# Kernel tuning notes

Measured on AMD Instinct MI355X. Metric: run time of the kernel, lower is better.

The kernel has to match this reference:

```python
import jax, jax.numpy as jnp
import numpy as np

SHAPE = 64
K = 8
HID = 512
OUT = K + 2 * K * SHAPE + 2 * SHAPE  # 1160
B, T = 32, 2048


def setup_inputs() -> dict:
    key = jax.random.key(0)
    ks = jax.random.split(key, 4)
    x = jax.random.normal(ks[0], (B, T, SHAPE), dtype=jnp.float32)
    W1 = jax.random.normal(ks[1], (SHAPE, HID), dtype=jnp.float32) / np.sqrt(SHAPE)
    b1 = jnp.zeros((HID,), dtype=jnp.float32)
    W2 = jax.random.normal(ks[2], (HID, HID), dtype=jnp.float32) / np.sqrt(HID)
    b2 = jnp.zeros((HID,), dtype=jnp.float32)
    W3 = jax.random.normal(ks[3], (HID, OUT), dtype=jnp.float32) / np.sqrt(HID) * 0.1
    b3 = jnp.zeros((OUT,), dtype=jnp.float32)
    return {"x": x, "W1": W1, "b1": b1, "W2": W2, "b2": b2, "W3": W3, "b3": b3}


def _coupling_forward(x, W1, b1, W2, b2, W3, b3):
    # coupling mask over feature dim: first half conditions the second half
    mask = jnp.zeros((SHAPE,), dtype=x.dtype).at[:SHAPE // 2].set(1.0)  # [D]
    x_ = x * mask  # [B,T,D]

    # conditioner MLP
    h = jax.nn.relu(x_ @ W1 + b1)
    h = jax.nn.relu(h @ W2 + b2)
    params = h @ W3 + b3  # [B,T,OUT]

    logscales = params[..., :SHAPE]
    biases = params[..., SHAPE:2 * SHAPE]
    mdn = params[..., 2 * SHAPE:]
    logits = mdn[..., :K]                                   # [B,T,K]
    mu = mdn[..., K:K + K * SHAPE].reshape(*x.shape[:2], K, SHAPE)
    logstd = mdn[..., K + K * SHAPE:].reshape(*x.shape[:2], K, SHAPE)

    # --- MixtureCDFFlow.flow ---
    weights = jax.nn.softmax(logits, axis=-1)[..., None]    # [B,T,K,1]
    std = jnp.exp(logstd)
    u = (x[:, :, None, :] - mu) / std                       # [B,T,K,D]
    cdf = 0.5 * (1.0 + jax.lax.erf(u / np.sqrt(2.0)))
    z = jnp.sum(cdf * weights, axis=2)                      # [B,T,D]
    pdf = jnp.exp(-0.5 * u * u) / (std * np.sqrt(2.0 * np.pi))
    logd_mix = jnp.log(jnp.sum(pdf * weights, axis=2))      # [B,T,D]

    # --- Inverse(Sigmoid).flow == Sigmoid.invert ---
    xs = -jnp.log(1.0 / z - 1.0)
    logd_sig = -jnp.log(z) - jnp.log(1.0 - z)

    # --- ElemwiseAffine.flow ---
    out = xs * jnp.exp(logscales) + biases
    log_det = logd_mix + logd_sig + logscales

    x_out = (1.0 - mask) * out + x_
    log_det = log_det * (1.0 - mask)
    return x_out, log_det


def reference(x, W1, b1, W2, b2, W3, b3):
    return _coupling_forward(x, W1, b1, W2, b2, W3, b3)
```

## Files before the change

kernel.cpp:

```cpp
#include <hip/hip_runtime.h>

typedef short short8 __attribute__((ext_vector_type(8)));
typedef float f32x4 __attribute__((ext_vector_type(4)));

#define NROWS 65536
#define NCOMPACT 640

__device__ __forceinline__ short f2bf(float f) {
  union { float f; unsigned u; } c; c.f = f;
  unsigned r = (c.u + 0x7fffu + ((c.u >> 16) & 1u)) >> 16;
  return (short)r;
}

__device__ __forceinline__ float fastrcp(float a) {
  float r; asm("v_rcp_f32 %0, %1" : "=v"(r) : "v"(a)); return r;
}

__device__ __forceinline__ int w3col(int n) {
  if (n < 32)  return 32 + n;
  if (n < 64)  return 96 + (n - 32);
  if (n < 72)  return 128 + (n - 64);
  if (n < 96)  return -1;
  if (n < 352) { int q = n - 96;  return 168 + (q >> 5) * 64 + (q & 31); }
  if (n < 608) { int q = n - 352; return 680 + (q >> 5) * 64 + (q & 31); }
  return -1;
}

__global__ __launch_bounds__(256) void prep_x_kernel(const float* __restrict__ x,
                                                     short* __restrict__ xc) {
  int t = blockIdx.x * 256 + threadIdx.x;
  if (t >= NROWS * 4) return;
  int row = t >> 2, seg = t & 3;
  const float* src = x + (size_t)row * 64 + seg * 8;
  short8 v;
#pragma unroll
  for (int i = 0; i < 8; ++i) v[i] = f2bf(src[i]);
  *(short8*)(xc + (size_t)row * 32 + seg * 8) = v;
}

__global__ __launch_bounds__(256) void prep_w_kernel(
    const float* __restrict__ W1, const float* __restrict__ W2,
    const float* __restrict__ W3, const float* __restrict__ b3,
    short* __restrict__ w1t, short* __restrict__ w2t,
    short* __restrict__ w3t, float* __restrict__ b3c) {
  const int NW1 = 512 * 32, NW2 = 512 * 512, NW3 = NCOMPACT * 512;
  int t = blockIdx.x * 256 + threadIdx.x;
  if (t < NW1) {
    int n = t >> 5, k = t & 31;
    w1t[t] = f2bf(W1[k * 512 + n]);
  } else if (t < NW1 + NW2) {
    int i = t - NW1; int n = i >> 9, k = i & 511;
    w2t[i] = f2bf(W2[k * 512 + n]);
  } else if (t < NW1 + NW2 + NW3) {
    int i = t - NW1 - NW2; int n = i >> 9, k = i & 511;
    int c = w3col(n);
    w3t[i] = (c >= 0) ? f2bf(W3[(size_t)k * 1160 + c]) : (short)0;
  } else if (t < NW1 + NW2 + NW3 + NCOMPACT) {
    int n = t - NW1 - NW2 - NW3;
    int c = w3col(n);
    b3c[n] = (c >= 0) ? b3[c] : 0.0f;
  }
}

template <int BK, int NT, bool RELU, bool OUT_BF16>
__global__ __launch_bounds__(256) void gemm_kernel(
    const short* __restrict__ A, const short* __restrict__ B,
    const float* __restrict__ bias, void* __restrict__ C, int K, int N) {
  __shared__ short As[128 * BK];
  __shared__ short Bs[128 * BK];
  const int tid = threadIdx.x;
  const int cpx = gridDim.x >> 3;
  const int s = blockIdx.x;
  const int w = (s & 7) * cpx + (s >> 3);
  const int m0 = (w / NT) * 128, n0 = (w % NT) * 128;
  const int lane = tid & 63, wid = tid >> 6;
  const int wm = (wid >> 1) * 64, wn = (wid & 1) * 64;
  const int lr = lane & 15, lk = (lane >> 4) * 8;
  constexpr int CPR = BK / 8;
  constexpr int SWM = CPR - 1;
  constexpr int NCHUNK = 128 * CPR;

  f32x4 acc[4][4] = {};

  for (int kt = 0; kt < K; kt += BK) {
    for (int base = wid * 64; base < NCHUNK; base += 256) {
      int c = base + lane;
      int row = c / CPR;
      int kb = (c % CPR) << 4;
      int skb = kb ^ ((row & SWM) << 4);
      const char* ga = (const char*)(A + (size_t)(m0 + row) * K + kt) + skb;
      const char* gb = (const char*)(B + (size_t)(n0 + row) * K + kt) + skb;
      __builtin_amdgcn_global_load_lds(
          (const __attribute__((address_space(1))) void*)ga,
          (__attribute__((address_space(3))) void*)((char*)As + (size_t)base * 16), 16, 0, 0);
      __builtin_amdgcn_global_load_lds(
          (const __attribute__((address_space(1))) void*)gb,
          (__attribute__((address_space(3))) void*)((char*)Bs + (size_t)base * 16), 16, 0, 0);
    }
    __syncthreads();
#pragma unroll
    for (int ks = 0; ks < BK; ks += 32) {
      short8 af[4], bf_[4];
#pragma unroll
      for (int mi = 0; mi < 4; ++mi) {
        int row = wm + mi * 16 + lr;
        int k = (ks + lk) ^ ((row & SWM) << 3);
        af[mi] = *(const short8*)(&As[row * BK + k]);
      }
#pragma unroll
      for (int ni = 0; ni < 4; ++ni) {
        int row = wn + ni * 16 + lr;
        int k = (ks + lk) ^ ((row & SWM) << 3);
        bf_[ni] = *(const short8*)(&Bs[row * BK + k]);
      }
#pragma unroll
      for (int mi = 0; mi < 4; ++mi)
#pragma unroll
        for (int ni = 0; ni < 4; ++ni)
          acc[mi][ni] = __builtin_amdgcn_mfma_f32_16x16x32_bf16(
              af[mi], bf_[ni], acc[mi][ni], 0, 0, 0);
    }
    __syncthreads();
  }

#pragma unroll
  for (int ni = 0; ni < 4; ++ni) {
    int col = n0 + wn + ni * 16 + lr;
    float bv = bias[col];
#pragma unroll
    for (int mi = 0; mi < 4; ++mi) {
#pragma unroll
      for (int j = 0; j < 4; ++j) {
        int row = m0 + wm + mi * 16 + (lane >> 4) * 4 + j;
        float v = acc[mi][ni][j] + bv;
        if (RELU) v = fmaxf(v, 0.0f);
        if (OUT_BF16) ((short*)C)[(size_t)row * N + col] = f2bf(v);
        else          ((float*)C)[(size_t)row * N + col] = v;
      }
    }
  }
}

#define PSTR 644
#define BUF1 49152
__global__ __launch_bounds__(1024, 4) void gemm3_fused_kernel(
    const short* __restrict__ A,
    const short* __restrict__ Bw,
    const float* __restrict__ b3c,
    const float* __restrict__ x,
    float* __restrict__ out) {
  __shared__ __attribute__((aligned(16))) char lds[98304];
  const int tid = threadIdx.x;
  const int m0 = blockIdx.x * 128;
  const int lane = tid & 63, wid = tid >> 6;
  const int wr = wid >> 2, wc = wid & 3;
  const int lr = lane & 15, hi = lane >> 4, lk = hi * 8;

  f32x4 acc[2][10] = {};

  auto STAGE = [&](int bo, int kt) {
#pragma unroll
    for (int base = wid * 64; base < 3072; base += 1024) {
      int c = base + lane;
      char* dst = lds + bo + (size_t)base * 16;
      if (base < 512) {
        int row = c >> 2;
        int skb = ((c & 3) ^ ((row >> 1) & 3)) << 4;
        const char* ga = (const char*)(A + (size_t)(m0 + row) * 512 + kt) + skb;
        __builtin_amdgcn_global_load_lds(
            (const __attribute__((address_space(1))) void*)ga,
            (__attribute__((address_space(3))) void*)dst, 16, 0, 0);
      } else {
        int q = c - 512;
        int row = q >> 2;
        int skb = ((q & 3) ^ ((row >> 1) & 3)) << 4;
        const char* gb = (const char*)(Bw + (size_t)row * 512 + kt) + skb;
        __builtin_amdgcn_global_load_lds(
            (const __attribute__((address_space(1))) void*)gb,
            (__attribute__((address_space(3))) void*)dst, 16, 0, 0);
      }
    }
  };

  auto COMPUTE = [&](int bo) {
    const short* As = (const short*)(lds + bo);
    const short* Bs = (const short*)(lds + bo + 8192);
    short8 af[2];
#pragma unroll
    for (int mi = 0; mi < 2; ++mi) {
      int row = wr * 32 + mi * 16 + lr;
      int k = lk ^ (((row >> 1) & 3) << 3);
      af[mi] = *(const short8*)(&As[row * 32 + k]);
    }
#pragma unroll
    for (int ni = 0; ni < 10; ++ni) {
      int brow = wc * 160 + ni * 16 + lr;
      int k = lk ^ (((brow >> 1) & 3) << 3);
      short8 bf_ = *(const short8*)(&Bs[brow * 32 + k]);
      acc[0][ni] = __builtin_amdgcn_mfma_f32_16x16x32_bf16(af[0], bf_, acc[0][ni], 0, 0, 0);
      acc[1][ni] = __builtin_amdgcn_mfma_f32_16x16x32_bf16(af[1], bf_, acc[1][ni], 0, 0, 0);
    }
  };

  STAGE(0, 0);
  __syncthreads();
  for (int t = 0; t < 16; t += 2) {
    STAGE(BUF1, (t + 1) * 32);
    COMPUTE(0);
    __syncthreads();
    if (t < 14) STAGE(0, (t + 2) * 32);
    COMPUTE(BUF1);
    __syncthreads();
  }

  float* plds = (float*)lds;
  float* xo  = out;
  float* ldo = out + (size_t)NROWS * 64;
#pragma unroll
  for (int p = 0; p < 4; ++p) {
    if (p) __syncthreads();
    if (wr == p) {
#pragma unroll
      for (int mi = 0; mi < 2; ++mi) {
#pragma unroll
        for (int ni = 0; ni < 10; ++ni) {
          int col = wc * 160 + ni * 16 + lr;
          float bv = b3c[col];
#pragma unroll
          for (int j = 0; j < 4; ++j)
            plds[(mi * 16 + hi * 4 + j) * PSTR + col] = acc[mi][ni][j] + bv;
        }
      }
    }
    __syncthreads();
    {
      int rl = tid >> 5, j = tid & 31;
      const float* p_ = plds + rl * PSTR;
      int grow = m0 + p * 32 + rl;

      float lg[8];
#pragma unroll
      for (int k = 0; k < 8; ++k) lg[k] = p_[64 + k];
      float mx = lg[0];
#pragma unroll
      for (int k = 1; k < 8; ++k) mx = fmaxf(mx, lg[k]);
      float wgt[8], wsum = 0.0f;
#pragma unroll
      for (int k = 0; k < 8; ++k) { wgt[k] = __expf(lg[k] - mx); wsum += wgt[k]; }

      float xd = x[(size_t)grow * 64 + 32 + j];
      float zs = 0.0f, ps = 0.0f;
#pragma unroll
      for (int k = 0; k < 8; ++k) {
        float mu   = p_[96 + k * 32 + j];
        float lstd = p_[352 + k * 32 + j];
        float istd = __expf(-lstd);
        float u = (xd - mu) * istd;
        float x2 = 0.5f * u * u;
        float e  = __expf(-x2);
        ps += wgt[k] * e * istd;
        float ax = fabsf(u) * 0.70710678118654752f;
        float t_ = fastrcp(fmaf(0.5f, ax, 1.0f));
        float poly = -1.26551223f + t_*(1.00002368f + t_*(0.37409196f +
                     t_*(0.09678418f + t_*(-0.18628806f + t_*(0.27886807f +
                     t_*(-1.13520398f + t_*(1.48851587f + t_*(-0.82215223f +
                     t_*0.17087277f))))))));
        float erfc_half = 0.5f * t_ * __expf(poly - x2);
        float cdf = (u >= 0.0f) ? 1.0f - erfc_half : erfc_half;
        zs += wgt[k] * cdf;
      }
      float winv = fastrcp(wsum);
      float z  = zs * winv;
      float pm = ps * winv * 0.39894228040143268f;
      float logz = __logf(z), log1mz = __logf(1.0f - z);
      float ls = p_[j], bv = p_[32 + j];
      float outv = (logz - log1mz) * __expf(ls) + bv;
      float ld = __logf(pm) - logz - log1mz + ls;

      size_t base = (size_t)grow * 64;
      xo[base + j]       = x[base + j];
      xo[base + 32 + j]  = outv;
      ldo[base + j]      = 0.0f;
      ldo[base + 32 + j] = ld;
    }
  }
}

extern "C" void kernel_launch(void* const* d_in, const int* in_sizes, int n_in,
                              void* d_out, int out_size, void* d_ws, size_t ws_size,
                              hipStream_t stream) {
  const float* x  = (const float*)d_in[0];
  const float* W1 = (const float*)d_in[1];
  const float* b1 = (const float*)d_in[2];
  const float* W2 = (const float*)d_in[3];
  const float* b2 = (const float*)d_in[4];
  const float* W3 = (const float*)d_in[5];
  const float* b3 = (const float*)d_in[6];
  char* ws = (char*)d_ws;

  short* xc  = (short*)ws;
  short* h1  = (short*)(ws + 4194304);
  short* h2  = (short*)(ws + 71303168);
  short* w1t = (short*)(ws + 138412032);
  short* w2t = (short*)(ws + 138444800);
  short* w3t = (short*)(ws + 138969088);
  float* b3c = (float*)(ws + 139624448);
  float* out = (float*)d_out;

  prep_x_kernel<<<(NROWS * 4) / 256, 256, 0, stream>>>(x, xc);
  {
    int total = 512 * 32 + 512 * 512 + NCOMPACT * 512 + NCOMPACT;
    prep_w_kernel<<<(total + 255) / 256, 256, 0, stream>>>(W1, W2, W3, b3, w1t, w2t, w3t, b3c);
  }
  gemm_kernel<32, 4, true, true><<<2048, 256, 0, stream>>>(xc, w1t, b1, h1, 32, 512);
  gemm_kernel<64, 4, true, true><<<2048, 256, 0, stream>>>(h1, w2t, b2, h2, 512, 512);
  gemm3_fused_kernel<<<NROWS / 128, 1024, 0, stream>>>(h2, w3t, b3c, x, out);
}
```

Measured before the change: 145.2 us.

## Reshape warp tiling to 2x8 and pipeline GEMM3 with vmcnt waits

Changes the fused third GEMM's wave layout from 4x4 to 2x8, so each wave computes a 64x80 tile (4x5 MFMA fragments) instead of 32x160. The main loop now keeps two LDS stages in flight. It uses explicit vmcnt waits and raw s_barriers instead of __syncthreads, and wraps the MFMA section in s_setprio. The goal is to overlap global-to-LDS loads with MFMA work and rebalance LDS fragment reads. The catch is fragile hand-managed wait counts and a different accumulator register footprint.

```diff
diff --git a/kernel.cpp b/kernel.cpp
--- a/kernel.cpp
+++ b/kernel.cpp
@@ -142,7 +142,8 @@
 }
 
 #define PSTR 644
-#define BUF1 49152
+#define FB1 49152
+#define WAITV(n) asm volatile("s_waitcnt vmcnt(" #n ")" ::: "memory")
 __global__ __launch_bounds__(1024, 4) void gemm3_fused_kernel(
     const short* __restrict__ A,
     const short* __restrict__ Bw,
@@ -153,10 +154,10 @@
   const int tid = threadIdx.x;
   const int m0 = blockIdx.x * 128;
   const int lane = tid & 63, wid = tid >> 6;
-  const int wr = wid >> 2, wc = wid & 3;
+  const int wr = wid >> 3, wc = wid & 7;
   const int lr = lane & 15, hi = lane >> 4, lk = hi * 8;
 
-  f32x4 acc[2][10] = {};
+  f32x4 acc[4][5] = {};
 
   auto STAGE = [&](int bo, int kt) {
 #pragma unroll
@@ -185,33 +186,51 @@
   auto COMPUTE = [&](int bo) {
     const short* As = (const short*)(lds + bo);
     const short* Bs = (const short*)(lds + bo + 8192);
-    short8 af[2];
-#pragma unroll
-    for (int mi = 0; mi < 2; ++mi) {
-      int row = wr * 32 + mi * 16 + lr;
+    short8 af[4];
+#pragma unroll
+    for (int mi = 0; mi < 4; ++mi) {
+      int row = wr * 64 + mi * 16 + lr;
       int k = lk ^ (((row >> 1) & 3) << 3);
       af[mi] = *(const short8*)(&As[row * 32 + k]);
     }
-#pragma unroll
-    for (int ni = 0; ni < 10; ++ni) {
-      int brow = wc * 160 + ni * 16 + lr;
+    __builtin_amdgcn_s_setprio(1);
+#pragma unroll
+    for (int ni = 0; ni < 5; ++ni) {
+      int brow = wc * 80 + ni * 16 + lr;
       int k = lk ^ (((brow >> 1) & 3) << 3);
       short8 bf_ = *(const short8*)(&Bs[brow * 32 + k]);
-      acc[0][ni] = __builtin_amdgcn_mfma_f32_16x16x32_bf16(af[0], bf_, acc[0][ni], 0, 0, 0);
-      acc[1][ni] = __builtin_amdgcn_mfma_f32_16x16x32_bf16(af[1], bf_, acc[1][ni], 0, 0, 0);
-    }
+#pragma unroll
+      for (int mi = 0; mi < 4; ++mi)
+        acc[mi][ni] = __builtin_amdgcn_mfma_f32_16x16x32_bf16(
+            af[mi], bf_, acc[mi][ni], 0, 0, 0);
+    }
+    __builtin_amdgcn_s_setprio(0);
   };
 
   STAGE(0, 0);
+  STAGE(FB1, 32);
+  for (int t = 0; t < 14; ++t) {
+    WAITV(3);
+    __builtin_amdgcn_sched_barrier(0);
+    __builtin_amdgcn_s_barrier();
+    __builtin_amdgcn_sched_barrier(0);
+    COMPUTE((t & 1) ? FB1 : 0);
+    __builtin_amdgcn_sched_barrier(0);
+    __builtin_amdgcn_s_barrier();
+    __builtin_amdgcn_sched_barrier(0);
+    STAGE((t & 1) ? FB1 : 0, (t + 2) * 32);
+  }
+  WAITV(3);
+  __builtin_amdgcn_sched_barrier(0);
+  __builtin_amdgcn_s_barrier();
+  __builtin_amdgcn_sched_barrier(0);
+  COMPUTE(0);
+  WAITV(0);
+  __builtin_amdgcn_sched_barrier(0);
+  __builtin_amdgcn_s_barrier();
+  __builtin_amdgcn_sched_barrier(0);
+  COMPUTE(FB1);
   __syncthreads();
-  for (int t = 0; t < 16; t += 2) {
-    STAGE(BUF1, (t + 1) * 32);
-    COMPUTE(0);
-    __syncthreads();
-    if (t < 14) STAGE(0, (t + 2) * 32);
-    COMPUTE(BUF1);
-    __syncthreads();
-  }
 
   float* plds = (float*)lds;
   float* xo  = out;
@@ -219,16 +238,17 @@
 #pragma unroll
   for (int p = 0; p < 4; ++p) {
     if (p) __syncthreads();
-    if (wr == p) {
-#pragma unroll
-      for (int mi = 0; mi < 2; ++mi) {
-#pragma unroll
-        for (int ni = 0; ni < 10; ++ni) {
-          int col = wc * 160 + ni * 16 + lr;
+    if (wr == (p >> 1)) {
+#pragma unroll
+      for (int mi2 = 0; mi2 < 2; ++mi2) {
+#pragma unroll
+        for (int ni = 0; ni < 5; ++ni) {
+          int col = wc * 80 + ni * 16 + lr;
           float bv = b3c[col];
 #pragma unroll
           for (int j = 0; j < 4; ++j)
-            plds[(mi * 16 + hi * 4 + j) * PSTR + col] = acc[mi][ni][j] + bv;
+            plds[(mi2 * 16 + hi * 4 + j) * PSTR + col] =
+                acc[(p & 1) * 2 + mi2][ni][j] + bv;
         }
       }
     }
```

New measurement: 146.5 us. About the same (+0.9%).

## Fuse all three MLP layers and epilogue into one per-row-block megakernel

Applied to the files above, without the earlier changes.

Replaces the x-prep kernel, the two standalone GEMM kernels and the fused third GEMM with a single kernel. Each 64-row block converts x to bf16 in LDS, computes layer 1, keeps the hidden activations in swizzled LDS across layers 2 and 3, and streams weight tiles through double buffers. This removes the HBM round trips for the h1/h2 intermediates and several launches. In exchange each block uses about 148KB of LDS, so only one block fits per CU, and every block re-streams all the weights (with smaller M tiles), which lowers occupancy and reuse.

```diff
diff --git a/kernel.cpp b/kernel.cpp
--- a/kernel.cpp
+++ b/kernel.cpp
@@ -2,6 +2,7 @@
 
 typedef short short8 __attribute__((ext_vector_type(8)));
 typedef float f32x4 __attribute__((ext_vector_type(4)));
+typedef float f32x4v __attribute__((ext_vector_type(4)));
 
 #define NROWS 65536
 #define NCOMPACT 640
@@ -24,18 +25,6 @@
   if (n < 352) { int q = n - 96;  return 168 + (q >> 5) * 64 + (q & 31); }
   if (n < 608) { int q = n - 352; return 680 + (q >> 5) * 64 + (q & 31); }
   return -1;
-}
-
-__global__ __launch_bounds__(256) void prep_x_kernel(const float* __restrict__ x,
-                                                     short* __restrict__ xc) {
-  int t = blockIdx.x * 256 + threadIdx.x;
-  if (t >= NROWS * 4) return;
-  int row = t >> 2, seg = t & 3;
-  const float* src = x + (size_t)row * 64 + seg * 8;
-  short8 v;
-#pragma unroll
-  for (int i = 0; i < 8; ++i) v[i] = f2bf(src[i]);
-  *(short8*)(xc + (size_t)row * 32 + seg * 8) = v;
 }
 
 __global__ __launch_bounds__(256) void prep_w_kernel(
@@ -62,154 +51,152 @@
   }
 }
 
-template <int BK, int NT, bool RELU, bool OUT_BF16>
-__global__ __launch_bounds__(256) void gemm_kernel(
-    const short* __restrict__ A, const short* __restrict__ B,
-    const float* __restrict__ bias, void* __restrict__ C, int K, int N) {
-  __shared__ short As[128 * BK];
-  __shared__ short Bs[128 * BK];
+#define OFF_A 0
+#define OFF_B 4096
+#define OFF_C 45056
+#define OFF_H 86016
+#define PSTR 644
+
+__global__ __launch_bounds__(1024) void mega_kernel(
+    const float* __restrict__ x,
+    const short* __restrict__ w1t,
+    const float* __restrict__ b1,
+    const short* __restrict__ w2t,
+    const float* __restrict__ b2,
+    const short* __restrict__ w3t,
+    const float* __restrict__ b3c,
+    float* __restrict__ out) {
+  __shared__ __attribute__((aligned(16))) char lds[151552];
   const int tid = threadIdx.x;
-  const int cpx = gridDim.x >> 3;
-  const int s = blockIdx.x;
-  const int w = (s & 7) * cpx + (s >> 3);
-  const int m0 = (w / NT) * 128, n0 = (w % NT) * 128;
+  const int m0 = blockIdx.x * 64;
   const int lane = tid & 63, wid = tid >> 6;
-  const int wm = (wid >> 1) * 64, wn = (wid & 1) * 64;
-  const int lr = lane & 15, lk = (lane >> 4) * 8;
-  constexpr int CPR = BK / 8;
-  constexpr int SWM = CPR - 1;
-  constexpr int NCHUNK = 128 * CPR;
-
-  f32x4 acc[4][4] = {};
-
-  for (int kt = 0; kt < K; kt += BK) {
-    for (int base = wid * 64; base < NCHUNK; base += 256) {
+  const int wr = wid >> 3, wc = wid & 7;
+  const int lr = lane & 15, hi = lane >> 4, lk = hi * 8;
+  short* Hs = (short*)(lds + OFF_H);
+
+  auto STAGE_W = [&](int bo, const short* src, int stride, int kt, int nchunk) {
+    for (int base = wid * 64; base < nchunk; base += 1024) {
       int c = base + lane;
-      int row = c / CPR;
-      int kb = (c % CPR) << 4;
-      int skb = kb ^ ((row & SWM) << 4);
-      const char* ga = (const char*)(A + (size_t)(m0 + row) * K + kt) + skb;
-      const char* gb = (const char*)(B + (size_t)(n0 + row) * K + kt) + skb;
+      int row = c >> 2;
+      int skb = ((c & 3) ^ ((row >> 1) & 3)) << 4;
+      const char* g = (const char*)(src + (size_t)row * stride + kt) + skb;
       __builtin_amdgcn_global_load_lds(
-          (const __attribute__((address_space(1))) void*)ga,
-          (__attribute__((address_space(3))) void*)((char*)As + (size_t)base * 16), 16, 0, 0);
-      __builtin_amdgcn_global_load_lds(
-          (const __attribute__((address_space(1))) void*)gb,
-          (__attribute__((address_space(3))) void*)((char*)Bs + (size_t)base * 16), 16, 0, 0);
-    }
-    __syncthreads();
-#pragma unroll
-    for (int ks = 0; ks < BK; ks += 32) {
-      short8 af[4], bf_[4];
-#pragma unroll
-      for (int mi = 0; mi < 4; ++mi) {
-        int row = wm + mi * 16 + lr;
-        int k = (ks + lk) ^ ((row & SWM) << 3);
-        af[mi] = *(const short8*)(&As[row * BK + k]);
-      }
-#pragma unroll
-      for (int ni = 0; ni < 4; ++ni) {
-        int row = wn + ni * 16 + lr;
-        int k = (ks + lk) ^ ((row & SWM) << 3);
-        bf_[ni] = *(const short8*)(&Bs[row * BK + k]);
-      }
-#pragma unroll
-      for (int mi = 0; mi < 4; ++mi)
-#pragma unroll
-        for (int ni = 0; ni < 4; ++ni)
-          acc[mi][ni] = __builtin_amdgcn_mfma_f32_16x16x32_bf16(
-              af[mi], bf_[ni], acc[mi][ni], 0, 0, 0);
-    }
-    __syncthreads();
-  }
-
-#pragma unroll
-  for (int ni = 0; ni < 4; ++ni) {
-    int col = n0 + wn + ni * 16 + lr;
-    float bv = bias[col];
-#pragma unroll
-    for (int mi = 0; mi < 4; ++mi) {
-#pragma unroll
-      for (int j = 0; j < 4; ++j) {
-        int row = m0 + wm + mi * 16 + (lane >> 4) * 4 + j;
-        float v = acc[mi][ni][j] + bv;
-        if (RELU) v = fmaxf(v, 0.0f);
-        if (OUT_BF16) ((short*)C)[(size_t)row * N + col] = f2bf(v);
-        else          ((float*)C)[(size_t)row * N + col] = v;
-      }
-    }
-  }
-}
-
-#define PSTR 644
-#define BUF1 49152
-__global__ __launch_bounds__(1024, 4) void gemm3_fused_kernel(
-    const short* __restrict__ A,
-    const short* __restrict__ Bw,
-    const float* __restrict__ b3c,
-    const float* __restrict__ x,
-    float* __restrict__ out) {
-  __shared__ __attribute__((aligned(16))) char lds[98304];
-  const int tid = threadIdx.x;
-  const int m0 = blockIdx.x * 128;
-  const int lane = tid & 63, wid = tid >> 6;
-  const int wr = wid >> 2, wc = wid & 3;
-  const int lr = lane & 15, hi = lane >> 4, lk = hi * 8;
-
-  f32x4 acc[2][10] = {};
-
-  auto STAGE = [&](int bo, int kt) {
-#pragma unroll
-    for (int base = wid * 64; base < 3072; base += 1024) {
-      int c = base + lane;
-      char* dst = lds + bo + (size_t)base * 16;
-      if (base < 512) {
-        int row = c >> 2;
-        int skb = ((c & 3) ^ ((row >> 1) & 3)) << 4;
-        const char* ga = (const char*)(A + (size_t)(m0 + row) * 512 + kt) + skb;
-        __builtin_amdgcn_global_load_lds(
-            (const __attribute__((address_space(1))) void*)ga,
-            (__attribute__((address_space(3))) void*)dst, 16, 0, 0);
-      } else {
-        int q = c - 512;
-        int row = q >> 2;
-        int skb = ((q & 3) ^ ((row >> 1) & 3)) << 4;
-        const char* gb = (const char*)(Bw + (size_t)row * 512 + kt) + skb;
-        __builtin_amdgcn_global_load_lds(
-            (const __attribute__((address_space(1))) void*)gb,
-            (__attribute__((address_space(3))) void*)dst, 16, 0, 0);
-      }
+          (const __attribute__((address_space(1))) void*)g,
+          (__attribute__((address_space(3))) void*)(lds + bo + (size_t)base * 16),
+          16, 0, 0);
     }
   };
 
-  auto COMPUTE = [&](int bo) {
-    const short* As = (const short*)(lds + bo);
-    const short* Bs = (const short*)(lds + bo + 8192);
+  if (tid < 256) {
+    int row = tid >> 2, seg = tid & 3;
+    const float* src = x + (size_t)(m0 + row) * 64 + seg * 8;
+    f32x4 v0 = *(const f32x4*)src;
+    f32x4 v1 = *(const f32x4*)(src + 4);
+    short8 v;
+#pragma unroll
+    for (int i = 0; i < 4; ++i) { v[i] = f2bf(v0[i]); v[4 + i] = f2bf(v1[i]); }
+    int sseg = seg ^ ((row >> 1) & 3);
+    *(short8*)(lds + OFF_A + row * 64 + sseg * 16) = v;
+  }
+  STAGE_W(OFF_B, w1t, 32, 0, 2048);
+  __syncthreads();
+
+  {
+    const short* As = (const short*)(lds + OFF_A);
+    const short* Ws = (const short*)(lds + OFF_B);
+    f32x4 acc1[2][4] = {};
     short8 af[2];
 #pragma unroll
     for (int mi = 0; mi < 2; ++mi) {
       int row = wr * 32 + mi * 16 + lr;
-      int k = lk ^ (((row >> 1) & 3) << 3);
-      af[mi] = *(const short8*)(&As[row * 32 + k]);
-    }
-#pragma unroll
-    for (int ni = 0; ni < 10; ++ni) {
-      int brow = wc * 160 + ni * 16 + lr;
-      int k = lk ^ (((brow >> 1) & 3) << 3);
-      short8 bf_ = *(const short8*)(&Bs[brow * 32 + k]);
-      acc[0][ni] = __builtin_amdgcn_mfma_f32_16x16x32_bf16(af[0], bf_, acc[0][ni], 0, 0, 0);
-      acc[1][ni] = __builtin_amdgcn_mfma_f32_16x16x32_bf16(af[1], bf_, acc[1][ni], 0, 0, 0);
-    }
-  };
-
-  STAGE(0, 0);
+      af[mi] = *(const short8*)(&As[row * 32 + (lk ^ (((row >> 1) & 3) << 3))]);
+    }
+#pragma unroll
+    for (int ni = 0; ni < 4; ++ni) {
+      int brow = wc * 64 + ni * 16 + lr;
+      short8 bf_ = *(const short8*)(&Ws[brow * 32 + (lk ^ (((brow >> 1) & 3) << 3))]);
+      acc1[0][ni] = __builtin_amdgcn_mfma_f32_16x16x32_bf16(af[0], bf_, acc1[0][ni], 0, 0, 0);
+      acc1[1][ni] = __builtin_amdgcn_mfma_f32_16x16x32_bf16(af[1], bf_, acc1[1][ni], 0, 0, 0);
+    }
+#pragma unroll
+    for (int ni = 0; ni < 4; ++ni) {
+      int col = wc * 64 + ni * 16 + lr;
+      float bv = b1[col];
+#pragma unroll
+      for (int mi = 0; mi < 2; ++mi) {
+#pragma unroll
+        for (int j = 0; j < 4; ++j) {
+          int row = wr * 32 + mi * 16 + hi * 4 + j;
+          float v = fmaxf(acc1[mi][j >= 0 ? ni : ni][j] + bv, 0.0f);
+          Hs[row * 512 + (col ^ ((row & 7) << 3))] = f2bf(v);
+        }
+      }
+    }
+  }
+  STAGE_W(OFF_C, w2t, 512, 0, 2048);
   __syncthreads();
-  for (int t = 0; t < 16; t += 2) {
-    STAGE(BUF1, (t + 1) * 32);
-    COMPUTE(0);
-    __syncthreads();
-    if (t < 14) STAGE(0, (t + 2) * 32);
-    COMPUTE(BUF1);
+
+  {
+    f32x4 acc2[2][4] = {};
+    for (int t = 0; t < 16; ++t) {
+      int buf  = (t & 1) ? OFF_B : OFF_C;
+      if (t < 15) STAGE_W((t & 1) ? OFF_C : OFF_B, w2t, 512, (t + 1) * 32, 2048);
+      const short* Ws = (const short*)(lds + buf);
+      short8 af[2];
+#pragma unroll
+      for (int mi = 0; mi < 2; ++mi) {
+        int row = wr * 32 + mi * 16 + lr;
+        af[mi] = *(const short8*)(&Hs[row * 512 + ((t * 32 + lk) ^ ((row & 7) << 3))]);
+      }
+      __builtin_amdgcn_s_setprio(1);
+#pragma unroll
+      for (int ni = 0; ni < 4; ++ni) {
+        int brow = wc * 64 + ni * 16 + lr;
+        short8 bf_ = *(const short8*)(&Ws[brow * 32 + (lk ^ (((brow >> 1) & 3) << 3))]);
+        acc2[0][ni] = __builtin_amdgcn_mfma_f32_16x16x32_bf16(af[0], bf_, acc2[0][ni], 0, 0, 0);
+        acc2[1][ni] = __builtin_amdgcn_mfma_f32_16x16x32_bf16(af[1], bf_, acc2[1][ni], 0, 0, 0);
+      }
+      __builtin_amdgcn_s_setprio(0);
+      __syncthreads();
+    }
+#pragma unroll
+    for (int ni = 0; ni < 4; ++ni) {
+      int col = wc * 64 + ni * 16 + lr;
+      float bv = b2[col];
+#pragma unroll
+      for (int mi = 0; mi < 2; ++mi) {
+#pragma unroll
+        for (int j = 0; j < 4; ++j) {
+          int row = wr * 32 + mi * 16 + hi * 4 + j;
+          float v = fmaxf(acc2[mi][ni][j] + bv, 0.0f);
+          Hs[row * 512 + (col ^ ((row & 7) << 3))] = f2bf(v);
+        }
+      }
+    }
+  }
+  STAGE_W(OFF_C, w3t, 512, 0, 2560);
+  __syncthreads();
+
+  f32x4 acc3[2][5] = {};
+  for (int t = 0; t < 16; ++t) {
+    int buf = (t & 1) ? OFF_B : OFF_C;
+    if (t < 15) STAGE_W((t & 1) ? OFF_C : OFF_B, w3t, 512, (t + 1) * 32, 2560);
+    const short* Ws = (const short*)(lds + buf);
+    short8 af[2];
+#pragma unroll
+    for (int mi = 0; mi < 2; ++mi) {
+      int row = wr * 32 + mi * 16 + lr;
+      af[mi] = *(const short8*)(&Hs[row * 512 + ((t * 32 + lk) ^ ((row & 7) << 3))]);
+    }
+    __builtin_amdgcn_s_setprio(1);
+#pragma unroll
+    for (int ni = 0; ni < 5; ++ni) {
+      int brow = wc * 80 + ni * 16 + lr;
+      short8 bf_ = *(const short8*)(&Ws[brow * 32 + (lk ^ (((brow >> 1) & 3) << 3))]);
+      acc3[0][ni] = __builtin_amdgcn_mfma_f32_16x16x32_bf16(af[0], bf_, acc3[0][ni], 0, 0, 0);
+      acc3[1][ni] = __builtin_amdgcn_mfma_f32_16x16x32_bf16(af[1], bf_, acc3[1][ni], 0, 0, 0);
+    }
+    __builtin_amdgcn_s_setprio(0);
     __syncthreads();
   }
 
@@ -217,18 +204,18 @@
   float* xo  = out;
   float* ldo = out + (size_t)NROWS * 64;
 #pragma unroll
-  for (int p = 0; p < 4; ++p) {
+  for (int p = 0; p < 2; ++p) {
     if (p) __syncthreads();
     if (wr == p) {
 #pragma unroll
-      for (int mi = 0; mi < 2; ++mi) {
-#pragma unroll
-        for (int ni = 0; ni < 10; ++ni) {
-          int col = wc * 160 + ni * 16 + lr;
+      for (int mi2 = 0; mi2 < 2; ++mi2) {
+#pragma unroll
+        for (int ni = 0; ni < 5; ++ni) {
+          int col = wc * 80 + ni * 16 + lr;
           float bv = b3c[col];
 #pragma unroll
           for (int j = 0; j < 4; ++j)
-            plds[(mi * 16 + hi * 4 + j) * PSTR + col] = acc[mi][ni][j] + bv;
+            plds[(mi2 * 16 + hi * 4 + j) * PSTR + col] = acc3[mi2][ni][j] + bv;
         }
       }
     }
@@ -298,21 +285,15 @@
   const float* b3 = (const float*)d_in[6];
   char* ws = (char*)d_ws;
 
-  short* xc  = (short*)ws;
-  short* h1  = (short*)(ws + 4194304);
-  short* h2  = (short*)(ws + 71303168);
-  short* w1t = (short*)(ws + 138412032);
-  short* w2t = (short*)(ws + 138444800);
-  short* w3t = (short*)(ws + 138969088);
-  float* b3c = (float*)(ws + 139624448);
+  short* w1t = (short*)ws;
+  short* w2t = (short*)(ws + 32768);
+  short* w3t = (short*)(ws + 557056);
+  float* b3c = (float*)(ws + 1212416);
   float* out = (float*)d_out;
 
-  prep_x_kernel<<<(NROWS * 4) / 256, 256, 0, stream>>>(x, xc);
   {
     int total = 512 * 32 + 512 * 512 + NCOMPACT * 512 + NCOMPACT;
     prep_w_kernel<<<(total + 255) / 256, 256, 0, stream>>>(W1, W2, W3, b3, w1t, w2t, w3t, b3c);
   }
-  gemm_kernel<32, 4, true, true><<<2048, 256, 0, stream>>>(xc, w1t, b1, h1, 32, 512);
-  gemm_kernel<64, 4, true, true><<<2048, 256, 0, stream>>>(h1, w2t, b2, h2, 512, 512);
-  gemm3_fused_kernel<<<NROWS / 128, 1024, 0, stream>>>(h2, w3t, b3c, x, out);
-}
+  mega_kernel<<<NROWS / 64, 1024, 0, stream>>>(x, w1t, b1, w2t, b2, w3t, b3c, out);
+}
```

Measured after the change: 161.8 us. +11.5%, slower.

## Fuse first MLP layer and input conversion into the second GEMM kernel

Applied to the files above, without the earlier changes.

Replaces the separate x-to-bf16 prep kernel and the layer-1 GEMM with on-the-fly computation inside the layer-2 GEMM. Each block converts its x rows to bf16 in registers and computes a 128x32 slice of h1 per k-step with MFMA, writing it straight into shared memory as the A operand. The 64MB h1 intermediate round-trip through global memory and two launches go away. W2 and W1 tiles are double-buffered. The cost is that h1 is recomputed by each of the four column tiles, and the k-step shrinks from 64 to 32, which adds barriers.

```diff
diff --git a/kernel.cpp b/kernel.cpp
--- a/kernel.cpp
+++ b/kernel.cpp
@@ -24,18 +24,6 @@
   if (n < 352) { int q = n - 96;  return 168 + (q >> 5) * 64 + (q & 31); }
   if (n < 608) { int q = n - 352; return 680 + (q >> 5) * 64 + (q & 31); }
   return -1;
-}
-
-__global__ __launch_bounds__(256) void prep_x_kernel(const float* __restrict__ x,
-                                                     short* __restrict__ xc) {
-  int t = blockIdx.x * 256 + threadIdx.x;
-  if (t >= NROWS * 4) return;
-  int row = t >> 2, seg = t & 3;
-  const float* src = x + (size_t)row * 64 + seg * 8;
-  short8 v;
-#pragma unroll
-  for (int i = 0; i < 8; ++i) v[i] = f2bf(src[i]);
-  *(short8*)(xc + (size_t)row * 32 + seg * 8) = v;
 }
 
 __global__ __launch_bounds__(256) void prep_w_kernel(
@@ -62,80 +50,136 @@
   }
 }
 
-template <int BK, int NT, bool RELU, bool OUT_BF16>
-__global__ __launch_bounds__(256) void gemm_kernel(
-    const short* __restrict__ A, const short* __restrict__ B,
-    const float* __restrict__ bias, void* __restrict__ C, int K, int N) {
-  __shared__ short As[128 * BK];
-  __shared__ short Bs[128 * BK];
+__global__ __launch_bounds__(256) void g12_kernel(
+    const float* __restrict__ x,
+    const short* __restrict__ w1t,
+    const float* __restrict__ b1,
+    const short* __restrict__ w2t,
+    const float* __restrict__ b2,
+    short* __restrict__ h2) {
+  __shared__ __attribute__((aligned(16))) short As[128 * 32];
+  __shared__ __attribute__((aligned(16))) short Bs[2][128 * 32];
+  __shared__ __attribute__((aligned(16))) short W1b[2][32 * 32];
   const int tid = threadIdx.x;
   const int cpx = gridDim.x >> 3;
   const int s = blockIdx.x;
   const int w = (s & 7) * cpx + (s >> 3);
-  const int m0 = (w / NT) * 128, n0 = (w % NT) * 128;
+  const int m0 = (w >> 2) * 128, n0 = (w & 3) * 128;
   const int lane = tid & 63, wid = tid >> 6;
   const int wm = (wid >> 1) * 64, wn = (wid & 1) * 64;
-  const int lr = lane & 15, lk = (lane >> 4) * 8;
-  constexpr int CPR = BK / 8;
-  constexpr int SWM = CPR - 1;
-  constexpr int NCHUNK = 128 * CPR;
+  const int lr = lane & 15, hi = lane >> 4, lk = hi * 8;
+
+  short8 xcf[2];
+#pragma unroll
+  for (int mi = 0; mi < 2; ++mi) {
+    int row = m0 + wid * 32 + mi * 16 + lr;
+    const float* xs = x + (size_t)row * 64 + lk;
+    f32x4 v0 = *(const f32x4*)xs;
+    f32x4 v1 = *(const f32x4*)(xs + 4);
+    short8 v;
+#pragma unroll
+    for (int i = 0; i < 4; ++i) { v[i] = f2bf(v0[i]); v[4 + i] = f2bf(v1[i]); }
+    xcf[mi] = v;
+  }
+
+  auto STAGE_B = [&](int buf, int kt) {
+#pragma unroll
+    for (int base = wid * 64; base < 512; base += 256) {
+      int c = base + lane;
+      int row = c >> 2;
+      int skb = ((c & 3) ^ (row & 3)) << 4;
+      const char* g = (const char*)(w2t + (size_t)(n0 + row) * 512 + kt) + skb;
+      __builtin_amdgcn_global_load_lds(
+          (const __attribute__((address_space(1))) void*)g,
+          (__attribute__((address_space(3))) void*)((char*)Bs[buf] + base * 16),
+          16, 0, 0);
+    }
+  };
+  auto STAGE_W1 = [&](int buf, int kt) {
+    if (wid < 2) {
+      int c = wid * 64 + lane;
+      int row = c >> 2;
+      int skb = ((c & 3) ^ (row & 3)) << 4;
+      const char* g = (const char*)(w1t + (size_t)(kt + row) * 32) + skb;
+      __builtin_amdgcn_global_load_lds(
+          (const __attribute__((address_space(1))) void*)g,
+          (__attribute__((address_space(3))) void*)((char*)W1b[buf] + wid * 1024),
+          16, 0, 0);
+    }
+  };
+
+  auto H1STEP = [&](int buf, int kt) {
+    const short* Wb = W1b[buf];
+    short8 wf[2];
+#pragma unroll
+    for (int ni = 0; ni < 2; ++ni) {
+      int row = ni * 16 + lr;
+      wf[ni] = *(const short8*)(&Wb[row * 32 + (lk ^ ((row & 3) << 3))]);
+    }
+    f32x4 a1[2][2] = {};
+#pragma unroll
+    for (int mi = 0; mi < 2; ++mi)
+#pragma unroll
+      for (int ni = 0; ni < 2; ++ni)
+        a1[mi][ni] = __builtin_amdgcn_mfma_f32_16x16x32_bf16(
+            xcf[mi], wf[ni], a1[mi][ni], 0, 0, 0);
+#pragma unroll
+    for (int ni = 0; ni < 2; ++ni) {
+      int acol = ni * 16 + lr;
+      float bv = b1[kt + acol];
+#pragma unroll
+      for (int mi = 0; mi < 2; ++mi)
+#pragma unroll
+        for (int j = 0; j < 4; ++j) {
+          int arow = wid * 32 + mi * 16 + hi * 4 + j;
+          int sc = (acol & 7) + ((((acol >> 3) ^ arow) & 3) << 3);
+          As[arow * 32 + sc] = f2bf(fmaxf(a1[mi][ni][j] + bv, 0.0f));
+        }
+    }
+  };
 
   f32x4 acc[4][4] = {};
-
-  for (int kt = 0; kt < K; kt += BK) {
-    for (int base = wid * 64; base < NCHUNK; base += 256) {
-      int c = base + lane;
-      int row = c / CPR;
-      int kb = (c % CPR) << 4;
-      int skb = kb ^ ((row & SWM) << 4);
-      const char* ga = (const char*)(A + (size_t)(m0 + row) * K + kt) + skb;
-      const char* gb = (const char*)(B + (size_t)(n0 + row) * K + kt) + skb;
-      __builtin_amdgcn_global_load_lds(
-          (const __attribute__((address_space(1))) void*)ga,
-          (__attribute__((address_space(3))) void*)((char*)As + (size_t)base * 16), 16, 0, 0);
-      __builtin_amdgcn_global_load_lds(
-          (const __attribute__((address_space(1))) void*)gb,
-          (__attribute__((address_space(3))) void*)((char*)Bs + (size_t)base * 16), 16, 0, 0);
-    }
-    __syncthreads();
-#pragma unroll
-    for (int ks = 0; ks < BK; ks += 32) {
-      short8 af[4], bf_[4];
-#pragma unroll
-      for (int mi = 0; mi < 4; ++mi) {
-        int row = wm + mi * 16 + lr;
-        int k = (ks + lk) ^ ((row & SWM) << 3);
-        af[mi] = *(const short8*)(&As[row * BK + k]);
-      }
-#pragma unroll
-      for (int ni = 0; ni < 4; ++ni) {
-        int row = wn + ni * 16 + lr;
-        int k = (ks + lk) ^ ((row & SWM) << 3);
-        bf_[ni] = *(const short8*)(&Bs[row * BK + k]);
-      }
-#pragma unroll
-      for (int mi = 0; mi < 4; ++mi)
-#pragma unroll
-        for (int ni = 0; ni < 4; ++ni)
-          acc[mi][ni] = __builtin_amdgcn_mfma_f32_16x16x32_bf16(
-              af[mi], bf_[ni], acc[mi][ni], 0, 0, 0);
-    }
+  auto COMPUTE = [&](int buf) {
+    short8 af[4], bf_[4];
+#pragma unroll
+    for (int mi = 0; mi < 4; ++mi) {
+      int row = wm + mi * 16 + lr;
+      af[mi] = *(const short8*)(&As[row * 32 + (lk ^ ((row & 3) << 3))]);
+    }
+#pragma unroll
+    for (int ni = 0; ni < 4; ++ni) {
+      int row = wn + ni * 16 + lr;
+      bf_[ni] = *(const short8*)(&Bs[buf][row * 32 + (lk ^ ((row & 3) << 3))]);
+    }
+#pragma unroll
+    for (int mi = 0; mi < 4; ++mi)
+#pragma unroll
+      for (int ni = 0; ni < 4; ++ni)
+        acc[mi][ni] = __builtin_amdgcn_mfma_f32_16x16x32_bf16(
+            af[mi], bf_[ni], acc[mi][ni], 0, 0, 0);
+  };
+
+  STAGE_B(0, 0); STAGE_W1(0, 0);
+  __syncthreads();
+  for (int t = 0; t < 16; ++t) {
+    int pb = t & 1;
+    if (t < 15) { STAGE_B(pb ^ 1, (t + 1) * 32); STAGE_W1(pb ^ 1, (t + 1) * 32); }
+    H1STEP(pb, t * 32);
+    __syncthreads();
+    COMPUTE(pb);
     __syncthreads();
   }
 
 #pragma unroll
   for (int ni = 0; ni < 4; ++ni) {
     int col = n0 + wn + ni * 16 + lr;
-    float bv = bias[col];
+    float bv = b2[col];
 #pragma unroll
     for (int mi = 0; mi < 4; ++mi) {
 #pragma unroll
       for (int j = 0; j < 4; ++j) {
-        int row = m0 + wm + mi * 16 + (lane >> 4) * 4 + j;
-        float v = acc[mi][ni][j] + bv;
-        if (RELU) v = fmaxf(v, 0.0f);
-        if (OUT_BF16) ((short*)C)[(size_t)row * N + col] = f2bf(v);
-        else          ((float*)C)[(size_t)row * N + col] = v;
+        int row = m0 + wm + mi * 16 + hi * 4 + j;
+        h2[(size_t)row * 512 + col] = f2bf(fmaxf(acc[mi][ni][j] + bv, 0.0f));
       }
     }
   }
@@ -298,21 +342,17 @@
   const float* b3 = (const float*)d_in[6];
   char* ws = (char*)d_ws;
 
-  short* xc  = (short*)ws;
-  short* h1  = (short*)(ws + 4194304);
-  short* h2  = (short*)(ws + 71303168);
-  short* w1t = (short*)(ws + 138412032);
-  short* w2t = (short*)(ws + 138444800);
-  short* w3t = (short*)(ws + 138969088);
-  float* b3c = (float*)(ws + 139624448);
+  short* h2  = (short*)ws;
+  short* w1t = (short*)(ws + 67108864);
+  short* w2t = (short*)(ws + 67141632);
+  short* w3t = (short*)(ws + 67665920);
+  float* b3c = (float*)(ws + 68321280);
   float* out = (float*)d_out;
 
-  prep_x_kernel<<<(NROWS * 4) / 256, 256, 0, stream>>>(x, xc);
   {
     int total = 512 * 32 + 512 * 512 + NCOMPACT * 512 + NCOMPACT;
     prep_w_kernel<<<(total + 255) / 256, 256, 0, stream>>>(W1, W2, W3, b3, w1t, w2t, w3t, b3c);
   }
-  gemm_kernel<32, 4, true, true><<<2048, 256, 0, stream>>>(xc, w1t, b1, h1, 32, 512);
-  gemm_kernel<64, 4, true, true><<<2048, 256, 0, stream>>>(h1, w2t, b2, h2, 512, 512);
+  g12_kernel<<<2048, 256, 0, stream>>>(x, w1t, b1, w2t, b2, h2);
   gemm3_fused_kernel<<<NROWS / 128, 1024, 0, stream>>>(h2, w3t, b3c, x, out);
 }
```

Measured after the change: 138.9 us. 1.04x faster.
